# Optimization experiments

Hardware: AMD Instinct MI355X
Metric: run time of the kernel (lower is better)

## Reference

```python
import jax, jax.numpy as jnp
import numpy as np

BS, C, H, W = 16, 64, 128, 128
NC = 80          # num classes (hardcoded 80 in original via expand(-1, 80, -1))
TOPK = 128
TAU = 0.07
EPS = 1e-12      # F.normalize eps


def setup_inputs() -> dict:
    key = jax.random.key(0)
    k1, k2, k3, k4 = jax.random.split(key, 4)
    feat = jax.random.normal(k1, (BS, C, H, W), dtype=jnp.float32)
    score = jax.random.uniform(k2, (BS, NC, H, W), dtype=jnp.float32)
    # hm: GT heatmap with exactly one 1.0 peak per (batch, class) for ~half the classes
    pos = jax.random.randint(k3, (BS, NC), 0, H * W)
    present = jax.random.bernoulli(k4, 0.5, (BS, NC)).astype(jnp.float32)
    b = jnp.arange(BS)[:, None]
    c = jnp.arange(NC)[None, :]
    hm = jnp.zeros((BS, NC, H * W), jnp.float32).at[b, c, pos].set(present)
    hm = hm.reshape(BS, NC, H, W)
    return {"feat": feat, "score": score, "hm": hm}


def reference(feat, score, hm):
    bs, c, h, w = feat.shape
    nc = hm.shape[1]
    hw = h * w
    score = jax.lax.stop_gradient(score)  # score.detach()

    # F.normalize(feat, dim=1)
    feat = feat / jnp.maximum(jnp.linalg.norm(feat, axis=1, keepdims=True), EPS)

    # q: feature at the hm==1 peak of each present class (one peak per (b,cls))
    peak = (hm == 1.0).astype(feat.dtype)                       # [bs,nc,h,w]
    q = jnp.einsum('bnhw,bchw->bnc', peak, feat)                # [bs,nc,c]
    class_mask = (peak.sum(axis=(2, 3)) > 0).astype(feat.dtype)  # [bs,nc]

    # k0: hm-weighted pooled feature per class, L2-normalized
    k0 = jnp.einsum('bchw,bnhw->bnc', feat, hm)                 # [bs,nc,c]
    k0 = k0 / jnp.maximum(jnp.linalg.norm(k0, axis=-1, keepdims=True), EPS)

    # mask score: zero at GT locations and for absent classes
    hm_free = (hm.sum(axis=1) == 0).astype(score.dtype)         # [bs,h,w]
    score = score * hm_free[:, None] * class_mask[:, :, None, None]

    max_values = score.max(axis=1).reshape(bs, hw)              # [bs,hw]
    class_indices = score.argmax(axis=1).reshape(bs, hw)        # [bs,hw]
    topk_values, topk_indices = jax.lax.top_k(max_values, TOPK)  # [bs,topk]
    k_all_mask_t = (topk_values > 0).astype(feat.dtype)         # [bs,topk]
    topk_class = jnp.take_along_axis(class_indices, topk_indices, axis=1)  # [bs,topk]

    feat_flat = feat.reshape(bs, c, hw)
    k_top = jnp.take_along_axis(feat_flat, topk_indices[:, None, :], axis=2)  # [bs,c,topk]
    k_top = k_top.transpose(0, 2, 1)                            # [bs,topk,c]

    # pseudo heatmap: 0.9 at selected (class, pos) pairs with positive score
    b_idx = jnp.arange(bs)[:, None]
    pseudo_hm = jnp.zeros((bs, nc, hw), feat.dtype).at[
        b_idx, topk_class, topk_indices].set(k_all_mask_t * 0.9)
    pseudo_hm = pseudo_hm.reshape(bs, nc, h, w)

    # positive mask: selected positions whose pseudo class matches the query class
    class_ids = jnp.arange(nc, dtype=feat.dtype)
    target = jnp.where(class_mask[:, :, None] == 1, class_ids[None, :, None], -1.0)  # [bs,nc,1]
    k_mask_top = (target == topk_class[:, None, :].astype(feat.dtype)).astype(feat.dtype)
    k_mask_top = k_mask_top * k_all_mask_t[:, None, :]          # [bs,nc,topk]
    k0_mask = class_mask[:, :, None] * jnp.eye(nc, dtype=feat.dtype)  # [bs,nc,nc]

    k_all = jnp.concatenate([k_top, k0], axis=1)                # [bs,topk+nc,c]
    k_mask = jnp.concatenate([k_mask_top, k0_mask], axis=-1)    # [bs,nc,topk+nc]
    k_all_mask = jnp.concatenate([k_all_mask_t, class_mask], axis=-1)  # [bs,topk+nc]

    sim = jnp.exp(jnp.einsum('bnc,bkc->bnk', q, k_all) / TAU)   # [bs,nc,topk+nc]
    sim_sum = (sim * k_all_mask[:, None, :]).sum(-1, keepdims=True)
    sim_sum = jnp.where(sim_sum == 0, 1.0, sim_sum)
    logit = jnp.where(k_mask > 0, sim / sim_sum, 1.0)
    log_loss = (jnp.log(logit) * k_mask).sum(-1)                # [bs,nc]
    num = k_mask.sum(-1)
    num = jnp.where(num == 0, 1.0, num)
    count = class_mask.sum()
    loss = ((log_loss / num) * class_mask).sum() / count
    return (-loss, pseudo_hm)
```

## Files before the change

kernel.cpp:

```cpp
#include <hip/hip_runtime.h>
#include <math.h>

#define BS 16
#define C 64
#define H 128
#define W 128
#define HW (H*W)
#define NC 80
#define TOPK 128
#define KALL (TOPK+NC)
#define TAU 0.07f
#define EPSN 1e-12f
#define OUT_N 20971521
#define GBLK (BS*KALL/4)
#define Z1BLK 1024
#define Z2BLK 1024
#define Z3BLK 256

__global__ __launch_bounds__(256) void k_peak_z(const float* __restrict__ hm,
                                                int* __restrict__ peak_pos,
                                                float* __restrict__ out) {
    int t = threadIdx.x;
    if (blockIdx.x >= BS * NC) {
        int zb = blockIdx.x - BS * NC;
        float4* o4 = (float4*)out;
        float4 z = make_float4(0.f, 0.f, 0.f, 0.f);
        int base = zb * 2048;
        #pragma unroll
        for (int j = 0; j < 8; ++j) o4[base + j * 256 + t] = z;
        return;
    }
    __shared__ int wmax[4];
    int bn = blockIdx.x;
    int lane = t & 63, wid = t >> 6;
    const float4* p = (const float4*)(hm + (size_t)bn * HW);
    int found = -1;
    #pragma unroll
    for (int j = 0; j < 16; ++j) {
        int gi = j * 256 + t;
        float4 v = p[gi];
        int base = gi * 4;
        if (v.x == 1.0f) found = base;
        if (v.y == 1.0f) found = base + 1;
        if (v.z == 1.0f) found = base + 2;
        if (v.w == 1.0f) found = base + 3;
    }
    #pragma unroll
    for (int off = 1; off < 64; off <<= 1) found = max(found, __shfl_xor(found, off));
    if (lane == 0) wmax[wid] = found;
    __syncthreads();
    if (t == 0) {
        int m = max(max(wmax[0], wmax[1]), max(wmax[2], wmax[3]));
        peak_pos[bn] = m;
    }
}

__global__ __launch_bounds__(256) void k_max_z(const float* __restrict__ score,
                                               const int* __restrict__ peak_pos,
                                               float* __restrict__ maxv,
                                               int* __restrict__ clsidx,
                                               float* __restrict__ out) {
    int t = threadIdx.x;
    if (blockIdx.x >= 256) {
        int zb = blockIdx.x - 256;
        float4* o4 = (float4*)out;
        float4 z = make_float4(0.f, 0.f, 0.f, 0.f);
        int base = 2097152 + zb * 2048;
        #pragma unroll
        for (int j = 0; j < 8; ++j) o4[base + j * 256 + t] = z;
        return;
    }
    __shared__ int pk[NC];
    int b = blockIdx.x >> 4;
    int g = (blockIdx.x & 15) * 256 + t;
    if (t < NC) pk[t] = peak_pos[b * NC + t];
    __syncthreads();
    const float4* sb = (const float4*)(score + (size_t)b * NC * HW);
    int p0 = g * 4;
    int pp0 = pk[0];
    float m0 = (pp0 >= 0) ? 1.0f : 0.0f;
    float4 v0 = sb[g];
    float bx = v0.x * m0, by = v0.y * m0, bz = v0.z * m0, bw = v0.w * m0;
    int ix = 0, iy = 0, iz = 0, iw = 0;
    bool pe0 = (pp0 == p0), pe1 = (pp0 == p0 + 1), pe2 = (pp0 == p0 + 2), pe3 = (pp0 == p0 + 3);
    #pragma unroll 8
    for (int n = 1; n < NC; ++n) {
        int pp = pk[n];
        float m = (pp >= 0) ? 1.0f : 0.0f;
        float4 v = sb[(size_t)n * (HW / 4) + g];
        float vx = v.x * m, vy = v.y * m, vz = v.z * m, vw = v.w * m;
        if (vx > bx) { bx = vx; ix = n; }
        if (vy > by) { by = vy; iy = n; }
        if (vz > bz) { bz = vz; iz = n; }
        if (vw > bw) { bw = vw; iw = n; }
        pe0 |= (pp == p0); pe1 |= (pp == p0 + 1); pe2 |= (pp == p0 + 2); pe3 |= (pp == p0 + 3);
    }
    if (pe0) { bx = 0.0f; ix = 0; }
    if (pe1) { by = 0.0f; iy = 0; }
    if (pe2) { bz = 0.0f; iz = 0; }
    if (pe3) { bw = 0.0f; iw = 0; }
    ((float4*)maxv)[(size_t)b * (HW / 4) + g] = make_float4(bx, by, bz, bw);
    ((int4*)clsidx)[(size_t)b * (HW / 4) + g] = make_int4(ix, iy, iz, iw);
}

__global__ __launch_bounds__(1024) void k_topk_z(const float* __restrict__ maxv,
                                                 const int* __restrict__ clsidx,
                                                 float* __restrict__ topkv,
                                                 int* __restrict__ topki,
                                                 int* __restrict__ topkc,
                                                 float* __restrict__ out) {
    int t = threadIdx.x;
    if (blockIdx.x >= BS) {
        int zb = blockIdx.x - BS;
        float4* o4 = (float4*)out;
        float4 z = make_float4(0.f, 0.f, 0.f, 0.f);
        int base = 4194304 + zb * 4096;
        #pragma unroll
        for (int j = 0; j < 4; ++j) o4[base + j * 1024 + t] = z;
        if (zb == 0 && t == 0) out[OUT_N - 1] = 0.0f;
        return;
    }
    __shared__ unsigned int hist[2048];
    __shared__ unsigned int wtot[16];
    __shared__ unsigned int woff[16];
    __shared__ unsigned int s_pref;
    __shared__ int s_rank;
    __shared__ unsigned int s_bin;
    __shared__ unsigned int s_above;

    int b = blockIdx.x;
    int lane = t & 63, wid = t >> 6;

    unsigned int key[16];
    const float4* mv4 = (const float4*)(maxv + (size_t)b * HW);
    #pragma unroll
    for (int j4 = 0; j4 < 4; ++j4) {
        float4 v = mv4[t * 4 + j4];
        key[j4 * 4 + 0] = __float_as_uint(v.x);
        key[j4 * 4 + 1] = __float_as_uint(v.y);
        key[j4 * 4 + 2] = __float_as_uint(v.z);
        key[j4 * 4 + 3] = __float_as_uint(v.w);
    }

    if (t == 0) { s_pref = 0u; s_rank = TOPK; }

    const int shifts[3] = {21, 10, 0};
    const int widths[3] = {11, 11, 10};

    for (int rnd = 0; rnd < 3; ++rnd) {
        int sh = shifts[rnd], w = widths[rnd];
        unsigned mask = (1u << w) - 1u;
        hist[t] = 0u; hist[t + 1024] = 0u;
        __syncthreads();
        unsigned pref = s_pref;
        int hiShift = sh + w;
        #pragma unroll
        for (int j = 0; j < 16; ++j) {
            unsigned k = key[j];
            bool ok = (rnd == 0) || ((k >> hiShift) == pref);
            if (ok) atomicAdd(&hist[(k >> sh) & mask], 1u);
        }
        __syncthreads();
        unsigned p = hist[2 * t] + hist[2 * t + 1];
        unsigned s = p;
        #pragma unroll
        for (int off = 1; off < 64; off <<= 1) {
            unsigned o = __shfl_down(s, off);
            if (lane + off < 64) s += o;
        }
        if (lane == 0) wtot[wid] = s;
        __syncthreads();
        if (wid == 0) {
            unsigned vv = (lane < 16) ? wtot[lane] : 0u;
            unsigned ss = vv;
            #pragma unroll
            for (int off = 1; off < 64; off <<= 1) {
                unsigned o = __shfl_down(ss, off);
                if (lane + off < 64) ss += o;
            }
            if (lane < 16) woff[lane] = ss - vv;
        }
        __syncthreads();
        unsigned S_t = s + woff[wid];
        unsigned S_next = S_t - p;
        int r = s_rank;
        if ((int)S_t >= r && (int)S_next < r) {
            unsigned hi = hist[2 * t + 1];
            if ((int)(S_next + hi) >= r) { s_bin = 2u * t + 1u; s_above = S_next; }
            else                         { s_bin = 2u * t;      s_above = S_next + hi; }
        }
        __syncthreads();
        if (t == 0) {
            s_pref = (s_pref << w) | s_bin;
            s_rank = s_rank - (int)s_above;
        }
        __syncthreads();
    }
    unsigned K = s_pref;
    int need_eq = s_rank;
    int cnt_gt = TOPK - need_eq;

    int cg = 0, ce = 0;
    #pragma unroll
    for (int j = 0; j < 16; ++j) { cg += (key[j] > K); ce += (key[j] == K); }
    unsigned v = ((unsigned)cg << 16) | (unsigned)ce;
    unsigned sc = v;
    #pragma unroll
    for (int off = 1; off < 64; off <<= 1) {
        unsigned o = __shfl_up(sc, off);
        if (lane >= off) sc += o;
    }
    if (lane == 63) wtot[wid] = sc;
    __syncthreads();
    if (wid == 0) {
        unsigned vv = (lane < 16) ? wtot[lane] : 0u;
        unsigned ss = vv;
        #pragma unroll
        for (int off = 1; off < 64; off <<= 1) {
            unsigned o = __shfl_up(ss, off);
            if (lane >= off) ss += o;
        }
        if (lane < 16) woff[lane] = ss - vv;
    }
    __syncthreads();
    unsigned ex = (sc - v) + woff[wid];
    int pg = (int)(ex >> 16);
    int pe = (int)(ex & 0xffffu);
    int lg = 0, le = 0;
    #pragma unroll
    for (int j = 0; j < 16; ++j) {
        unsigned k = key[j];
        int slot = -1;
        if (k > K) { slot = pg + lg; ++lg; }
        else if (k == K) { int er = pe + le; ++le; if (er < need_eq) slot = cnt_gt + er; }
        if (slot >= 0) {
            int idx = t * 16 + j;
            topkv[b * TOPK + slot] = __uint_as_float(k);
            topki[b * TOPK + slot] = idx;
            topkc[b * TOPK + slot] = clsidx[(size_t)b * HW + idx];
        }
    }
}

__global__ __launch_bounds__(256) void k_gather_sc(const float* __restrict__ feat,
                                                   const int* __restrict__ peak_pos,
                                                   const float* __restrict__ topkv,
                                                   const int* __restrict__ topki,
                                                   const int* __restrict__ topkc,
                                                   float* __restrict__ k_all,
                                                   float* __restrict__ qv,
                                                   float* __restrict__ out) {
    int t = threadIdx.x;
    if (blockIdx.x == GBLK) {
        #pragma unroll
        for (int j = 0; j < 8; ++j) {
            int i = j * 256 + t;
            if (topkv[i] > 0.0f) {
                int b = i >> 7;
                out[1 + (((size_t)b * NC + topkc[i]) << 14) + topki[i]] = 0.9f;
            }
        }
        return;
    }
    int wid = t >> 6, lane = t & 63;
    int bk = blockIdx.x * 4 + wid;
    int b = bk / KALL, k = bk % KALL, c = lane;
    int pos;
    if (k < TOPK) {
        pos = topki[b * TOPK + k];
    } else {
        int n = k - TOPK;
        int pp = peak_pos[b * NC + n];
        if (pp < 0) {
            k_all[((size_t)b * KALL + k) * C + c] = 0.0f;
            qv[((size_t)b * NC + n) * C + c] = 0.0f;
            return;
        }
        pos = pp;
    }
    float v = feat[((size_t)b * C + c) * HW + pos];
    float ss = v * v;
    #pragma unroll
    for (int off = 1; off < 64; off <<= 1) ss += __shfl_xor(ss, off);
    float qc = v / fmaxf(sqrtf(ss), EPSN);
    if (k < TOPK) {
        k_all[((size_t)b * KALL + k) * C + c] = qc;
    } else {
        int n = k - TOPK;
        qv[((size_t)b * NC + n) * C + c] = qc;
        float qq = qc * qc;
        #pragma unroll
        for (int off = 1; off < 64; off <<= 1) qq += __shfl_xor(qq, off);
        k_all[((size_t)b * KALL + k) * C + c] = qc / fmaxf(sqrtf(qq), EPSN);
    }
}

__global__ __launch_bounds__(256) void k_loss(const float* __restrict__ k_all,
                                              const float* __restrict__ qv,
                                              const int* __restrict__ peak_pos,
                                              const float* __restrict__ topkv,
                                              const int* __restrict__ topkc,
                                              float* __restrict__ loss_bn) {
    __shared__ float qs[C];
    __shared__ float r1[256];
    __shared__ float r2[256];
    __shared__ float s_simsum, s_num;
    int bn = blockIdx.x;
    int b = bn / NC, n = bn % NC, t = threadIdx.x;
    if (peak_pos[bn] < 0) { if (t == 0) loss_bn[bn] = 0.0f; return; }
    if (t < C) qs[t] = qv[(size_t)bn * C + t];
    __syncthreads();
    float sim = 0.0f, kam = 0.0f, km = 0.0f;
    if (t < KALL) {
        const float* kr = k_all + ((size_t)b * KALL + t) * C;
        float dot = 0.0f;
        for (int c2 = 0; c2 < C; ++c2) dot += qs[c2] * kr[c2];
        sim = expf(dot / TAU);
        if (t < TOPK) {
            float posm = (topkv[b * TOPK + t] > 0.0f) ? 1.0f : 0.0f;
            kam = posm;
            km = (topkc[b * TOPK + t] == n) ? posm : 0.0f;
        } else {
            int j = t - TOPK;
            kam = (peak_pos[b * NC + j] >= 0) ? 1.0f : 0.0f;
            km = (j == n) ? 1.0f : 0.0f;
        }
    }
    r1[t] = sim * kam;
    r2[t] = km;
    __syncthreads();
    for (int s = 128; s > 0; s >>= 1) {
        if (t < s) { r1[t] += r1[t + s]; r2[t] += r2[t + s]; }
        __syncthreads();
    }
    if (t == 0) {
        float ss = r1[0];
        s_simsum = (ss == 0.0f) ? 1.0f : ss;
        s_num = (r2[0] == 0.0f) ? 1.0f : r2[0];
    }
    __syncthreads();
    r1[t] = (km > 0.0f) ? logf(sim / s_simsum) : 0.0f;
    __syncthreads();
    for (int s = 128; s > 0; s >>= 1) {
        if (t < s) r1[t] += r1[t + s];
        __syncthreads();
    }
    if (t == 0) loss_bn[bn] = r1[0] / s_num;
}

__global__ __launch_bounds__(256) void k_final(const float* __restrict__ loss_bn,
                                               const int* __restrict__ peak_pos,
                                               float* __restrict__ out) {
    __shared__ float r1[256];
    __shared__ float r2[256];
    int t = threadIdx.x;
    float s = 0.0f, cnt = 0.0f;
    for (int i = t; i < BS * NC; i += 256) {
        s += loss_bn[i];
        cnt += (peak_pos[i] >= 0) ? 1.0f : 0.0f;
    }
    r1[t] = s; r2[t] = cnt;
    __syncthreads();
    for (int st = 128; st > 0; st >>= 1) {
        if (t < st) { r1[t] += r1[t + st]; r2[t] += r2[t + st]; }
        __syncthreads();
    }
    if (t == 0) out[0] = -(r1[0] / r2[0]);
}

extern "C" void kernel_launch(void* const* d_in, const int* in_sizes, int n_in,
                              void* d_out, int out_size, void* d_ws, size_t ws_size,
                              hipStream_t stream) {
    const float* feat  = (const float*)d_in[0];
    const float* score = (const float*)d_in[1];
    const float* hm    = (const float*)d_in[2];
    float* out = (float*)d_out;

    char* ws = (char*)d_ws;
    size_t off = 0;
    auto alloc = [&](size_t bytes) -> void* {
        void* p = ws + off;
        off += (bytes + 255) & ~(size_t)255;
        return p;
    };
    int*   peak_pos = (int*)  alloc((size_t)BS * NC * 4);
    float* maxv     = (float*)alloc((size_t)BS * HW * 4);
    int*   clsidx   = (int*)  alloc((size_t)BS * HW * 4);
    float* topkv    = (float*)alloc((size_t)BS * TOPK * 4);
    int*   topki    = (int*)  alloc((size_t)BS * TOPK * 4);
    int*   topkc    = (int*)  alloc((size_t)BS * TOPK * 4);
    float* k_all    = (float*)alloc((size_t)BS * KALL * C * 4);
    float* qv       = (float*)alloc((size_t)BS * NC * C * 4);
    float* loss_bn  = (float*)alloc((size_t)BS * NC * 4);

    k_peak_z<<<BS * NC + Z1BLK, 256, 0, stream>>>(hm, peak_pos, out);
    k_max_z<<<256 + Z2BLK, 256, 0, stream>>>(score, peak_pos, maxv, clsidx, out);
    k_topk_z<<<BS + Z3BLK, 1024, 0, stream>>>(maxv, clsidx, topkv, topki, topkc, out);
    k_gather_sc<<<GBLK + 1, 256, 0, stream>>>(feat, peak_pos, topkv, topki, topkc,
                                              k_all, qv, out);
    k_loss<<<BS * NC, 256, 0, stream>>>(k_all, qv, peak_pos, topkv, topkc, loss_bn);
    k_final<<<1, 256, 0, stream>>>(loss_bn, peak_pos, out);
}
```

Before: 100.2 us.

## Interleave output zero-fill into peak and max kernels instead of separate blocks

Removes the dedicated zero-fill blocks from the peak, max and topk kernels and spreads the pseudo_hm zeroing across the working threads. The peak kernel now runs 1024-thread blocks that each zero a slice while scanning hm, and the max kernel zeroes one slice every other class iteration. This is meant to overlap output stores with input reads and to free the topk kernel of zero work. It adds store traffic inside the bandwidth-bound loops and changes the peak kernel's block size and reduction width.

After: 99.90 us. Within noise of the previous version (-0.3%).

```diff
diff --git a/kernel.cpp b/kernel.cpp
--- a/kernel.cpp
+++ b/kernel.cpp
@@ -13,44 +13,55 @@
 #define EPSN 1e-12f
 #define OUT_N 20971521
 #define GBLK (BS*KALL/4)
-#define Z1BLK 1024
-#define Z2BLK 1024
-#define Z3BLK 256
-
-__global__ __launch_bounds__(256) void k_peak_z(const float* __restrict__ hm,
-                                                int* __restrict__ peak_pos,
-                                                float* __restrict__ out) {
-    int t = threadIdx.x;
-    if (blockIdx.x >= BS * NC) {
-        int zb = blockIdx.x - BS * NC;
-        float4* o4 = (float4*)out;
-        float4 z = make_float4(0.f, 0.f, 0.f, 0.f);
-        int base = zb * 2048;
-        #pragma unroll
-        for (int j = 0; j < 8; ++j) o4[base + j * 256 + t] = z;
-        return;
-    }
-    __shared__ int wmax[4];
-    int bn = blockIdx.x;
+#define HALF4 2621440
+
+__global__ __launch_bounds__(1024) void k_peak_z(const float* __restrict__ hm,
+                                                 int* __restrict__ peak_pos,
+                                                 float* __restrict__ out) {
+    __shared__ int wmax[16];
+    int bn = blockIdx.x, t = threadIdx.x;
     int lane = t & 63, wid = t >> 6;
     const float4* p = (const float4*)(hm + (size_t)bn * HW);
+    float4* o4 = (float4*)out;
+    const float4 z = make_float4(0.f, 0.f, 0.f, 0.f);
+    int zbase = bn * 2048 + t;
+    float4 v0 = p[t];
+    o4[zbase] = z;
+    float4 v1 = p[1024 + t];
+    o4[zbase + 1024] = z;
+    float4 v2 = p[2048 + t];
+    float4 v3 = p[3072 + t];
     int found = -1;
-    #pragma unroll
-    for (int j = 0; j < 16; ++j) {
-        int gi = j * 256 + t;
-        float4 v = p[gi];
-        int base = gi * 4;
-        if (v.x == 1.0f) found = base;
-        if (v.y == 1.0f) found = base + 1;
-        if (v.z == 1.0f) found = base + 2;
-        if (v.w == 1.0f) found = base + 3;
+    {
+        int b0 = t * 4;
+        if (v0.x == 1.0f) found = b0;
+        if (v0.y == 1.0f) found = b0 + 1;
+        if (v0.z == 1.0f) found = b0 + 2;
+        if (v0.w == 1.0f) found = b0 + 3;
+        int b1 = (1024 + t) * 4;
+        if (v1.x == 1.0f) found = b1;
+        if (v1.y == 1.0f) found = b1 + 1;
+        if (v1.z == 1.0f) found = b1 + 2;
+        if (v1.w == 1.0f) found = b1 + 3;
+        int b2 = (2048 + t) * 4;
+        if (v2.x == 1.0f) found = b2;
+        if (v2.y == 1.0f) found = b2 + 1;
+        if (v2.z == 1.0f) found = b2 + 2;
+        if (v2.w == 1.0f) found = b2 + 3;
+        int b3 = (3072 + t) * 4;
+        if (v3.x == 1.0f) found = b3;
+        if (v3.y == 1.0f) found = b3 + 1;
+        if (v3.z == 1.0f) found = b3 + 2;
+        if (v3.w == 1.0f) found = b3 + 3;
     }
     #pragma unroll
     for (int off = 1; off < 64; off <<= 1) found = max(found, __shfl_xor(found, off));
     if (lane == 0) wmax[wid] = found;
     __syncthreads();
     if (t == 0) {
-        int m = max(max(wmax[0], wmax[1]), max(wmax[2], wmax[3]));
+        int m = wmax[0];
+        #pragma unroll
+        for (int i = 1; i < 16; ++i) m = max(m, wmax[i]);
         peak_pos[bn] = m;
     }
 }
@@ -60,22 +71,16 @@
                                                float* __restrict__ maxv,
                                                int* __restrict__ clsidx,
                                                float* __restrict__ out) {
+    __shared__ int pk[NC];
     int t = threadIdx.x;
-    if (blockIdx.x >= 256) {
-        int zb = blockIdx.x - 256;
-        float4* o4 = (float4*)out;
-        float4 z = make_float4(0.f, 0.f, 0.f, 0.f);
-        int base = 2097152 + zb * 2048;
-        #pragma unroll
-        for (int j = 0; j < 8; ++j) o4[base + j * 256 + t] = z;
-        return;
-    }
-    __shared__ int pk[NC];
     int b = blockIdx.x >> 4;
     int g = (blockIdx.x & 15) * 256 + t;
+    int gt = blockIdx.x * 256 + t;
     if (t < NC) pk[t] = peak_pos[b * NC + t];
     __syncthreads();
     const float4* sb = (const float4*)(score + (size_t)b * NC * HW);
+    float4* o4 = (float4*)out;
+    const float4 z = make_float4(0.f, 0.f, 0.f, 0.f);
     int p0 = g * 4;
     int pp0 = pk[0];
     float m0 = (pp0 >= 0) ? 1.0f : 0.0f;
@@ -85,6 +90,7 @@
     bool pe0 = (pp0 == p0), pe1 = (pp0 == p0 + 1), pe2 = (pp0 == p0 + 2), pe3 = (pp0 == p0 + 3);
     #pragma unroll 8
     for (int n = 1; n < NC; ++n) {
+        if (n & 1) o4[HALF4 + ((n >> 1) * 65536) + gt] = z;
         int pp = pk[n];
         float m = (pp >= 0) ? 1.0f : 0.0f;
         float4 v = sb[(size_t)n * (HW / 4) + g];
@@ -101,25 +107,14 @@
     if (pe3) { bw = 0.0f; iw = 0; }
     ((float4*)maxv)[(size_t)b * (HW / 4) + g] = make_float4(bx, by, bz, bw);
     ((int4*)clsidx)[(size_t)b * (HW / 4) + g] = make_int4(ix, iy, iz, iw);
-}
-
-__global__ __launch_bounds__(1024) void k_topk_z(const float* __restrict__ maxv,
-                                                 const int* __restrict__ clsidx,
-                                                 float* __restrict__ topkv,
-                                                 int* __restrict__ topki,
-                                                 int* __restrict__ topkc,
-                                                 float* __restrict__ out) {
-    int t = threadIdx.x;
-    if (blockIdx.x >= BS) {
-        int zb = blockIdx.x - BS;
-        float4* o4 = (float4*)out;
-        float4 z = make_float4(0.f, 0.f, 0.f, 0.f);
-        int base = 4194304 + zb * 4096;
-        #pragma unroll
-        for (int j = 0; j < 4; ++j) o4[base + j * 1024 + t] = z;
-        if (zb == 0 && t == 0) out[OUT_N - 1] = 0.0f;
-        return;
-    }
+    if (gt == 0) out[OUT_N - 1] = 0.0f;
+}
+
+__global__ __launch_bounds__(1024) void k_topk(const float* __restrict__ maxv,
+                                               const int* __restrict__ clsidx,
+                                               float* __restrict__ topkv,
+                                               int* __restrict__ topki,
+                                               int* __restrict__ topkc) {
     __shared__ unsigned int hist[2048];
     __shared__ unsigned int wtot[16];
     __shared__ unsigned int woff[16];
@@ -128,7 +123,7 @@
     __shared__ unsigned int s_bin;
     __shared__ unsigned int s_above;
 
-    int b = blockIdx.x;
+    int b = blockIdx.x, t = threadIdx.x;
     int lane = t & 63, wid = t >> 6;
 
     unsigned int key[16];
@@ -393,9 +388,9 @@
     float* qv       = (float*)alloc((size_t)BS * NC * C * 4);
     float* loss_bn  = (float*)alloc((size_t)BS * NC * 4);
 
-    k_peak_z<<<BS * NC + Z1BLK, 256, 0, stream>>>(hm, peak_pos, out);
-    k_max_z<<<256 + Z2BLK, 256, 0, stream>>>(score, peak_pos, maxv, clsidx, out);
-    k_topk_z<<<BS + Z3BLK, 1024, 0, stream>>>(maxv, clsidx, topkv, topki, topkc, out);
+    k_peak_z<<<BS * NC, 1024, 0, stream>>>(hm, peak_pos, out);
+    k_max_z<<<256, 256, 0, stream>>>(score, peak_pos, maxv, clsidx, out);
+    k_topk<<<BS, 1024, 0, stream>>>(maxv, clsidx, topkv, topki, topkc);
     k_gather_sc<<<GBLK + 1, 256, 0, stream>>>(feat, peak_pos, topkv, topki, topkc,
                                               k_all, qv, out);
     k_loss<<<BS * NC, 256, 0, stream>>>(k_all, qv, peak_pos, topkv, topkc, loss_bn);
```
